# Performance work log

Measured on AMD Instinct MI355X. Metric: run time of the kernel, lower is better.

## Reference

```python
import jax, jax.numpy as jnp
import numpy as np

N_TAXON = 100000
N_SOTU = 200000
D = 128      # input feature dim and hidden_channels
OUT = 64     # out_channels
E_HP = 200000
E_RH = 2000000


def _sage(x_src, x_dst, src, dst, Wl, Wr, b, n_dst):
    # PyG SAGEConv (mean aggr): out = lin_l(mean_{j in N(i)} x_j) + lin_r(x_i)
    msgs = x_src[src]                                            # [E, d] gather
    summed = jax.ops.segment_sum(msgs, dst, num_segments=n_dst)  # [n_dst, d]
    cnt = jax.ops.segment_sum(jnp.ones_like(msgs[:, 0]), dst, num_segments=n_dst)
    mean = summed / jnp.maximum(cnt, 1.0)[:, None]
    return mean @ Wl + b + x_dst @ Wr


def setup_inputs() -> dict:
    key = jax.random.key(0)
    ks = jax.random.split(key, 20)
    s = 1.0 / np.sqrt(D)
    inp = {
        "x_taxon": jax.random.normal(ks[0], (N_TAXON, D), jnp.float32),
        "x_sotu": jax.random.normal(ks[1], (N_SOTU, D), jnp.float32),
        "edge_hp_src": jax.random.randint(ks[2], (E_HP,), 0, N_TAXON),
        "edge_hp_dst": jax.random.randint(ks[3], (E_HP,), 0, N_TAXON),
        "edge_rh_src": jax.random.randint(ks[4], (E_RH,), 0, N_TAXON),
        "edge_rh_dst": jax.random.randint(ks[5], (E_RH,), 0, N_SOTU),
        # conv1: taxon -> taxon
        "W1l": jax.random.normal(ks[6], (D, D), jnp.float32) * s,
        "W1r": jax.random.normal(ks[7], (D, D), jnp.float32) * s,
        "b1": jnp.zeros((D,), jnp.float32),
        # conv2: (taxon, sotu) bipartite
        "W2l": jax.random.normal(ks[8], (D, D), jnp.float32) * s,
        "W2r": jax.random.normal(ks[9], (D, D), jnp.float32) * s,
        "b2": jnp.zeros((D,), jnp.float32),
        # conv3: (taxon_hidden, sotu_hidden) bipartite
        "W3l": jax.random.normal(ks[10], (D, D), jnp.float32) * s,
        "W3r": jax.random.normal(ks[11], (D, D), jnp.float32) * s,
        "b3": jnp.zeros((D,), jnp.float32),
        # final linear
        "Wlin": jax.random.normal(ks[12], (D, OUT), jnp.float32) * s,
        "blin": jnp.zeros((OUT,), jnp.float32),
    }
    return inp


def reference(x_taxon, x_sotu, edge_hp_src, edge_hp_dst, edge_rh_src, edge_rh_dst,
              W1l, W1r, b1, W2l, W2r, b2, W3l, W3r, b3, Wlin, blin):
    taxon_h = jax.nn.relu(_sage(x_taxon, x_taxon, edge_hp_src, edge_hp_dst,
                                W1l, W1r, b1, N_TAXON))
    sotu_h = jax.nn.relu(_sage(x_taxon, x_sotu, edge_rh_src, edge_rh_dst,
                               W2l, W2r, b2, N_SOTU))
    sotu_h = jax.nn.relu(_sage(taxon_h, sotu_h, edge_rh_src, edge_rh_dst,
                               W3l, W3r, b3, N_SOTU))
    return sotu_h @ Wlin + blin
```

## Files before the change

kernel.cpp:

```cpp
#include <hip/hip_runtime.h>
#include <hip/hip_bf16.h>

#define D 128
#define N_TAXON 100000
#define N_SOTU 200000
#define E_HP 200000
#define E_RH 2000000
#define OUTC 64
#define NBUCK 98
#define BSHIFT 11

typedef __hip_bfloat16 bf16;
typedef __bf16 bf16v8 __attribute__((ext_vector_type(8)));
typedef float f32x4 __attribute__((ext_vector_type(4)));
typedef int i32x4 __attribute__((ext_vector_type(4)));
typedef unsigned u32x2 __attribute__((ext_vector_type(2)));

union Frag { i32x4 i; bf16v8 v; };

__device__ __forceinline__ float bflo(unsigned u) { return __uint_as_float(u << 16); }
__device__ __forceinline__ float bfhi(unsigned u) { return __uint_as_float(u & 0xffff0000u); }

__device__ __forceinline__ unsigned short f2bf(float x) {
    unsigned u = __float_as_uint(x);
    unsigned r = (u + 0x7fffu + ((u >> 16) & 1u)) >> 16;
    return (unsigned short)r;
}
__device__ __forceinline__ unsigned packbf(float a, float b) {
    return (unsigned)f2bf(a) | ((unsigned)f2bf(b) << 16);
}

__global__ __launch_bounds__(256) void countAll_kernel(const int* __restrict__ hp_dst,
                                                       const int* __restrict__ rh_dst,
                                                       unsigned* __restrict__ cnt_t,
                                                       unsigned* __restrict__ bcnt)
{
    __shared__ unsigned hist[NBUCK];
    if (threadIdx.x < NBUCK) hist[threadIdx.x] = 0;
    __syncthreads();
    int stride = gridDim.x * 256;
    for (int e = blockIdx.x * 256 + threadIdx.x; e < E_HP; e += stride)
        atomicAdd(&cnt_t[hp_dst[e]], 1u);
    for (int e = blockIdx.x * 256 + threadIdx.x; e < E_RH; e += stride)
        atomicAdd(&hist[rh_dst[e] >> BSHIFT], 1u);
    __syncthreads();
    if (threadIdx.x < NBUCK) atomicAdd(&bcnt[threadIdx.x], hist[threadIdx.x]);
}

__global__ __launch_bounds__(128) void scan98_kernel(const unsigned* __restrict__ bcnt,
                                                     unsigned* __restrict__ bcursor,
                                                     unsigned* __restrict__ bstart,
                                                     unsigned* __restrict__ row_ptr)
{
    __shared__ unsigned v[NBUCK];
    if (threadIdx.x < NBUCK) v[threadIdx.x] = bcnt[threadIdx.x];
    __syncthreads();
    if (threadIdx.x == 0) {
        unsigned acc = 0;
        for (int b = 0; b < NBUCK; ++b) {
            unsigned t = v[b];
            bcursor[b] = acc; bstart[b] = acc; acc += t;
        }
        bstart[NBUCK] = acc;
        row_ptr[N_TAXON + N_SOTU] = E_HP + acc;
    }
}

__global__ __launch_bounds__(256) void partition_kernel(
    const int* __restrict__ src, const int* __restrict__ dst,
    unsigned* __restrict__ bcursor, unsigned long long* __restrict__ ebuf, int n)
{
    __shared__ unsigned hist[NBUCK];
    __shared__ unsigned lcur[NBUCK];
    int base = blockIdx.x * 4096;
    if (threadIdx.x < NBUCK) hist[threadIdx.x] = 0;
    __syncthreads();
    int s[16], d[16];
#pragma unroll
    for (int k = 0; k < 16; ++k) {
        int e = base + k * 256 + threadIdx.x;
        if (e < n) {
            s[k] = src[e]; d[k] = dst[e];
            atomicAdd(&hist[d[k] >> BSHIFT], 1u);
        } else d[k] = -1;
    }
    __syncthreads();
    if (threadIdx.x < NBUCK)
        lcur[threadIdx.x] = atomicAdd(&bcursor[threadIdx.x], hist[threadIdx.x]);
    __syncthreads();
#pragma unroll
    for (int k = 0; k < 16; ++k) {
        if (d[k] >= 0) {
            unsigned slot = atomicAdd(&lcur[d[k] >> BSHIFT], 1u);
            ebuf[slot] = ((unsigned long long)(unsigned)d[k] << 32) | (unsigned)s[k];
        }
    }
}

__global__ __launch_bounds__(256) void scanA_kernel(const unsigned* __restrict__ cnt,
                                                    unsigned* __restrict__ bsum, int n)
{
    int lane = threadIdx.x & 63, wv = threadIdx.x >> 6;
    __shared__ unsigned ws[4];
    int i = blockIdx.x * 256 + threadIdx.x;
    unsigned v = (i < n) ? cnt[i] : 0u;
    for (int off = 1; off < 64; off <<= 1) v += __shfl_xor(v, off, 64);
    if (lane == 0) ws[wv] = v;
    __syncthreads();
    if (threadIdx.x == 0) bsum[blockIdx.x] = ws[0] + ws[1] + ws[2] + ws[3];
}

__global__ __launch_bounds__(1024) void scanB_kernel(unsigned* __restrict__ bsum, int nb,
                                                     unsigned* __restrict__ total_out)
{
    int lane = threadIdx.x & 63, wv = threadIdx.x >> 6;
    __shared__ unsigned wsum[16];
    int t = threadIdx.x;
    unsigned v0 = (2 * t     < nb) ? bsum[2 * t]     : 0u;
    unsigned v1 = (2 * t + 1 < nb) ? bsum[2 * t + 1] : 0u;
    unsigned v = v0 + v1;
    unsigned s = v;
    for (int off = 1; off < 64; off <<= 1) {
        unsigned tt = __shfl_up(s, off, 64);
        if (lane >= off) s += tt;
    }
    if (lane == 63) wsum[wv] = s;
    __syncthreads();
    unsigned woff = 0, tot = 0;
    for (int w = 0; w < 16; ++w) { if (w < wv) woff += wsum[w]; tot += wsum[w]; }
    unsigned ex = woff + s - v;
    if (2 * t     < nb) bsum[2 * t]     = ex;
    if (2 * t + 1 < nb) bsum[2 * t + 1] = ex + v0;
    if (t == 0) *total_out = tot;
}

__global__ __launch_bounds__(256) void scanC_kernel(const unsigned* __restrict__ cnt,
                                                    const unsigned* __restrict__ bsum,
                                                    unsigned* __restrict__ row_ptr,
                                                    unsigned* __restrict__ cursor, int n)
{
    int lane = threadIdx.x & 63, wv = threadIdx.x >> 6;
    __shared__ unsigned wsum[4];
    int i = blockIdx.x * 256 + threadIdx.x;
    unsigned v = (i < n) ? cnt[i] : 0u;
    unsigned s = v;
    for (int off = 1; off < 64; off <<= 1) {
        unsigned t = __shfl_up(s, off, 64);
        if (lane >= off) s += t;
    }
    if (lane == 63) wsum[wv] = s;
    __syncthreads();
    unsigned woff = bsum[blockIdx.x];
    for (int w = 0; w < wv; ++w) woff += wsum[w];
    if (i < n) { unsigned p = woff + s - v; row_ptr[i] = p; cursor[i] = p; }
}

__global__ __launch_bounds__(256) void fill_hp_kernel(const int* __restrict__ src,
                                                      const int* __restrict__ dst,
                                                      unsigned* __restrict__ cursor,
                                                      int* __restrict__ sorted_all)
{
    int stride = gridDim.x * 256;
    for (int i = blockIdx.x * 256 + threadIdx.x; i < E_HP; i += stride) {
        unsigned pos = atomicAdd(&cursor[dst[i]], 1u);
        sorted_all[pos] = src[i];
    }
}

__global__ __launch_bounds__(256) void fillB_kernel(const unsigned long long* __restrict__ ebuf,
                                                    const unsigned* __restrict__ bstart,
                                                    unsigned* __restrict__ row_ptr,
                                                    int* __restrict__ sorted_all)
{
    __shared__ unsigned hist[1 << BSHIFT];
    __shared__ unsigned wsum[4];
    int c = blockIdx.x;
    int dbase = c << BSHIFT;
    for (int i = threadIdx.x; i < (1 << BSHIFT); i += 256) hist[i] = 0;
    __syncthreads();
    unsigned e0 = bstart[c], e1 = bstart[c + 1];
    for (unsigned e = e0 + threadIdx.x; e < e1; e += 256)
        atomicAdd(&hist[(unsigned)(ebuf[e] >> 32) - dbase], 1u);
    __syncthreads();
    int base8 = threadIdx.x * 8;
    unsigned loc[8], s = 0;
#pragma unroll
    for (int i = 0; i < 8; ++i) { loc[i] = s; s += hist[base8 + i]; }
    int lane = threadIdx.x & 63, wv = threadIdx.x >> 6;
    unsigned sc = s;
    for (int off = 1; off < 64; off <<= 1) {
        unsigned t = __shfl_up(sc, off, 64);
        if (lane >= off) sc += t;
    }
    if (lane == 63) wsum[wv] = sc;
    __syncthreads();
    unsigned woff = 0;
    for (int w = 0; w < wv; ++w) woff += wsum[w];
    unsigned tbase = E_HP + e0 + woff + sc - s;
#pragma unroll
    for (int i = 0; i < 8; ++i) {
        int dd = dbase + base8 + i;
        unsigned p = tbase + loc[i];
        if (dd < N_SOTU) row_ptr[N_TAXON + dd] = p;
        hist[base8 + i] = p;
    }
    __syncthreads();
    for (unsigned e = e0 + threadIdx.x; e < e1; e += 256) {
        unsigned long long v = ebuf[e];
        unsigned pos = atomicAdd(&hist[(unsigned)(v >> 32) - dbase], 1u);
        sorted_all[pos] = (int)(unsigned)v;
    }
}

__global__ __launch_bounds__(256) void wprep_all_kernel(
    const float* __restrict__ W1l, const float* __restrict__ W1r,
    const float* __restrict__ W2l, const float* __restrict__ W2r,
    const float* __restrict__ W3l, const float* __restrict__ W3r,
    const float* __restrict__ Wlin, unsigned short* __restrict__ wtbase)
{
    int e = blockIdx.x * 256 + threadIdx.x;
    if (e >= 6 * 16384 + 8192) return;
    const float* srcs[7] = { W1l, W1r, W2l, W2r, W3l, W3r, Wlin };
    int m = e >> 14;
    int local = (m < 6) ? (e & 16383) : (e - 98304);
    int N = (m < 6) ? 128 : 64;
    int k = local / N, col = local - k * N;
    unsigned short* dst = wtbase + ((m < 6) ? m * 16384 : 98304);
    dst[(col * 128 + k) ^ ((col & 7) << 3)] = f2bf(srcs[m][local]);
}

__global__ __launch_bounds__(256) void aggMeanHp_kernel(
    const float* __restrict__ x, const unsigned* __restrict__ rp,
    const int* __restrict__ nbr, unsigned* __restrict__ outm)
{
    int wave = threadIdx.x >> 6, lane = threadIdx.x & 63;
    int bid = (blockIdx.x & 7) * 3125 + (blockIdx.x >> 3);
    int r = bid * 4 + wave;
    unsigned beg = rp[r], end = rp[r + 1];
    float a0 = 0.f, a1 = 0.f;
    unsigned u = beg;
    for (; u + 2 <= end; u += 2) {
        float2 A = ((const float2*)x)[(size_t)nbr[u] * 64 + lane];
        float2 B = ((const float2*)x)[(size_t)nbr[u + 1] * 64 + lane];
        a0 += A.x + B.x; a1 += A.y + B.y;
    }
    if (u < end) {
        float2 A = ((const float2*)x)[(size_t)nbr[u] * 64 + lane];
        a0 += A.x; a1 += A.y;
    }
    unsigned c = end - beg;
    float inv = 1.f / (float)(c ? c : 1u);
    outm[(size_t)r * 64 + lane] = packbf(a0 * inv, a1 * inv);
}

__global__ __launch_bounds__(1024) void gemmTh_kernel(
    const unsigned* __restrict__ A1 , const float* __restrict__ X ,
    const unsigned short* __restrict__ WtA, const unsigned short* __restrict__ WtB,
    const float* __restrict__ bias, unsigned* __restrict__ X2, int M)
{
    __shared__ char sW[65536];
    {
        int tid = threadIdx.x;
        ((i32x4*)sW)[tid]        = ((const i32x4*)WtA)[tid];
        ((i32x4*)sW)[tid + 1024] = ((const i32x4*)WtA)[tid + 1024];
        ((i32x4*)sW)[tid + 2048] = ((const i32x4*)WtB)[tid];
        ((i32x4*)sW)[tid + 3072] = ((const i32x4*)WtB)[tid + 1024];
    }
    __syncthreads();

    int wave = threadIdx.x >> 6, lane = threadIdx.x & 63;
    int ln = lane & 15, g = lane >> 4;
    int row = blockIdx.x * 256 + wave * 16 + ln;
    int rl = row < M ? row : M - 1;
    int swz = (ln & 7) << 4;

    f32x4 acc[8];
#pragma unroll
    for (int cf = 0; cf < 8; ++cf) acc[cf] = ((const f32x4*)bias)[cf * 4 + g];

    const i32x4* a1r = (const i32x4*)(A1 + (size_t)rl * 64);
    const f32x4* xr = (const f32x4*)(X + (size_t)rl * 128);
    unsigned* orow = X2 + (size_t)row * 128;
    i32x4 xpk[4];
#pragma unroll
    for (int ks = 0; ks < 4; ++ks) {
        Frag mf; mf.i = a1r[ks * 4 + g];
        f32x4 fa = xr[ks * 8 + g * 2], fb = xr[ks * 8 + g * 2 + 1];
        Frag xf;
        i32x4 t = { (int)packbf(fa.x, fa.y), (int)packbf(fa.z, fa.w),
                    (int)packbf(fb.x, fb.y), (int)packbf(fb.z, fb.w) };
        xf.i = t; xpk[ks] = t;
#pragma unroll
        for (int cf = 0; cf < 8; ++cf) {
            int off = (((cf * 16 + ln) << 8) + (ks << 6) + (g << 4)) ^ swz;
            Frag wa; wa.i = *(const i32x4*)(sW + off);
            Frag wb; wb.i = *(const i32x4*)(sW + 32768 + off);
            acc[cf] = __builtin_amdgcn_mfma_f32_16x16x32_bf16(wa.v, mf.v, acc[cf], 0, 0, 0);
            acc[cf] = __builtin_amdgcn_mfma_f32_16x16x32_bf16(wb.v, xf.v, acc[cf], 0, 0, 0);
        }
    }

    if (row < M) {
#pragma unroll
        for (int ks = 0; ks < 4; ++ks) {
            int p0 = 16 * ks + 4 * g;
            orow[(p0 + 0) * 2] = (unsigned)xpk[ks][0];
            orow[(p0 + 1) * 2] = (unsigned)xpk[ks][1];
            orow[(p0 + 2) * 2] = (unsigned)xpk[ks][2];
            orow[(p0 + 3) * 2] = (unsigned)xpk[ks][3];
        }
#pragma unroll
        for (int cf = 0; cf < 8; ++cf) {
            int p = cf * 8 + g * 2;
            orow[p * 2 + 1]       = packbf(fmaxf(acc[cf][0], 0.f), fmaxf(acc[cf][1], 0.f));
            orow[(p + 1) * 2 + 1] = packbf(fmaxf(acc[cf][2], 0.f), fmaxf(acc[cf][3], 0.f));
        }
    }
}

__global__ __launch_bounds__(256) void aggMean2_kernel(
    const unsigned* __restrict__ X2, const unsigned* __restrict__ rp,
    const int* __restrict__ nbr,
    unsigned* __restrict__ meanXrh, unsigned* __restrict__ meanH)
{
    int wave = threadIdx.x >> 6, lane = threadIdx.x & 63;
    int bid = (blockIdx.x & 7) * 6250 + (blockIdx.x >> 3);
    int r = bid * 4 + wave;
    unsigned beg = rp[r], end = rp[r + 1];
    float a0 = 0.f, a1 = 0.f, a2 = 0.f, a3 = 0.f;
    unsigned u = beg;
    for (; u + 2 <= end; u += 2) {
        int j0 = nbr[u], j1 = nbr[u + 1];
        u32x2 A = *(const u32x2*)(X2 + (size_t)j0 * 128 + lane * 2);
        u32x2 B = *(const u32x2*)(X2 + (size_t)j1 * 128 + lane * 2);
        a0 += bflo(A.x) + bflo(B.x); a1 += bfhi(A.x) + bfhi(B.x);
        a2 += bflo(A.y) + bflo(B.y); a3 += bfhi(A.y) + bfhi(B.y);
    }
    if (u < end) {
        u32x2 A = *(const u32x2*)(X2 + (size_t)nbr[u] * 128 + lane * 2);
        a0 += bflo(A.x); a1 += bfhi(A.x); a2 += bflo(A.y); a3 += bfhi(A.y);
    }
    unsigned c = end - beg;
    float inv = 1.f / (float)(c ? c : 1u);
    meanXrh[(size_t)r * 64 + lane] = packbf(a0 * inv, a1 * inv);
    meanH[(size_t)r * 64 + lane]   = packbf(a2 * inv, a3 * inv);
}

__global__ __launch_bounds__(1024) void megaTail_kernel(
    const unsigned* __restrict__ meanXrh, const float* __restrict__ xs,
    const unsigned* __restrict__ meanH,
    const unsigned short* __restrict__ Wt2l, const unsigned short* __restrict__ Wt2r,
    const unsigned short* __restrict__ Wt3l, const unsigned short* __restrict__ Wt3r,
    const unsigned short* __restrict__ Wtlin,
    const float* __restrict__ b2, const float* __restrict__ b3,
    const float* __restrict__ blin, float* __restrict__ out, int M)
{
    __shared__ char sW[65536];
    __shared__ unsigned tiles[16 * 1024];
    int tid = threadIdx.x;
    int wave = tid >> 6, lane = tid & 63;
    int ln = lane & 15, g = lane >> 4;
    int row = blockIdx.x * 256 + wave * 16 + ln;
    int rl = row < M ? row : M - 1;
    int swzW = (ln & 7) << 4;
    int swz = (ln & 7) << 2;
    unsigned* tile = tiles + wave * 1024;

    i32x4 w3pre[4], wlpre;
    w3pre[0] = ((const i32x4*)Wt3l)[tid];
    w3pre[1] = ((const i32x4*)Wt3l)[tid + 1024];
    w3pre[2] = ((const i32x4*)Wt3r)[tid];
    w3pre[3] = ((const i32x4*)Wt3r)[tid + 1024];
    wlpre    = ((const i32x4*)Wtlin)[tid];

    ((i32x4*)sW)[tid]        = ((const i32x4*)Wt2l)[tid];
    ((i32x4*)sW)[tid + 1024] = ((const i32x4*)Wt2l)[tid + 1024];
    ((i32x4*)sW)[tid + 2048] = ((const i32x4*)Wt2r)[tid];
    ((i32x4*)sW)[tid + 3072] = ((const i32x4*)Wt2r)[tid + 1024];
    __syncthreads();

    {
        f32x4 acc[8];
#pragma unroll
        for (int cf = 0; cf < 8; ++cf) acc[cf] = ((const f32x4*)b2)[cf * 4 + g];
        const i32x4* a1r = (const i32x4*)(meanXrh + (size_t)rl * 64);
        const f32x4* xr = (const f32x4*)(xs + (size_t)rl * 128);
#pragma unroll
        for (int ks = 0; ks < 4; ++ks) {
            Frag mf; mf.i = a1r[ks * 4 + g];
            f32x4 fa = xr[ks * 8 + g * 2], fb = xr[ks * 8 + g * 2 + 1];
            Frag xf;
            i32x4 t = { (int)packbf(fa.x, fa.y), (int)packbf(fa.z, fa.w),
                        (int)packbf(fb.x, fb.y), (int)packbf(fb.z, fb.w) };
            xf.i = t;
#pragma unroll
            for (int cf = 0; cf < 8; ++cf) {
                int off = (((cf * 16 + ln) << 8) + (ks << 6) + (g << 4)) ^ swzW;
                Frag wa; wa.i = *(const i32x4*)(sW + off);
                Frag wb; wb.i = *(const i32x4*)(sW + 32768 + off);
                acc[cf] = __builtin_amdgcn_mfma_f32_16x16x32_bf16(wa.v, mf.v, acc[cf], 0, 0, 0);
                acc[cf] = __builtin_amdgcn_mfma_f32_16x16x32_bf16(wb.v, xf.v, acc[cf], 0, 0, 0);
            }
        }
#pragma unroll
        for (int cf = 0; cf < 8; ++cf) {
            u32x2 o;
            o.x = packbf(fmaxf(acc[cf][0], 0.f), fmaxf(acc[cf][1], 0.f));
            o.y = packbf(fmaxf(acc[cf][2], 0.f), fmaxf(acc[cf][3], 0.f));
            *(u32x2*)&tile[ln * 64 + ((cf * 8 + g * 2) ^ swz)] = o;
        }
    }

    i32x4 mh[4];
    {
        const i32x4* hr = (const i32x4*)(meanH + (size_t)rl * 64);
#pragma unroll
        for (int ks = 0; ks < 4; ++ks) mh[ks] = hr[ks * 4 + g];
    }
    __syncthreads();
    ((i32x4*)sW)[tid]        = w3pre[0];
    ((i32x4*)sW)[tid + 1024] = w3pre[1];
    ((i32x4*)sW)[tid + 2048] = w3pre[2];
    ((i32x4*)sW)[tid + 3072] = w3pre[3];
    __syncthreads();

    {
        f32x4 acc2[8];
#pragma unroll
        for (int cf = 0; cf < 8; ++cf) acc2[cf] = ((const f32x4*)b3)[cf * 4 + g];
#pragma unroll
        for (int ks = 0; ks < 4; ++ks) {
            Frag mf; mf.i = mh[ks];
            Frag sf; sf.i = *(const i32x4*)&tile[ln * 64 + ((ks * 16 + g * 4) ^ swz)];
#pragma unroll
            for (int cf = 0; cf < 8; ++cf) {
                int off = (((cf * 16 + ln) << 8) + (ks << 6) + (g << 4)) ^ swzW;
                Frag wl; wl.i = *(const i32x4*)(sW + off);
                Frag wr; wr.i = *(const i32x4*)(sW + 32768 + off);
                acc2[cf] = __builtin_amdgcn_mfma_f32_16x16x32_bf16(wl.v, mf.v, acc2[cf], 0, 0, 0);
                acc2[cf] = __builtin_amdgcn_mfma_f32_16x16x32_bf16(wr.v, sf.v, acc2[cf], 0, 0, 0);
            }
        }
#pragma unroll
        for (int cf = 0; cf < 8; ++cf) {
            u32x2 o;
            o.x = packbf(fmaxf(acc2[cf][0], 0.f), fmaxf(acc2[cf][1], 0.f));
            o.y = packbf(fmaxf(acc2[cf][2], 0.f), fmaxf(acc2[cf][3], 0.f));
            *(u32x2*)&tile[ln * 64 + ((cf * 8 + g * 2) ^ swz)] = o;
        }
    }
    __syncthreads();
    ((i32x4*)sW)[tid] = wlpre;
    __syncthreads();

    f32x4 aL[4];
#pragma unroll
    for (int cf = 0; cf < 4; ++cf) aL[cf] = ((const f32x4*)blin)[cf * 4 + g];
#pragma unroll
    for (int ks = 0; ks < 4; ++ks) {
        Frag hf; hf.i = *(const i32x4*)&tile[ln * 64 + ((ks * 16 + g * 4) ^ swz)];
#pragma unroll
        for (int cf = 0; cf < 4; ++cf) {
            int off = (((cf * 16 + ln) << 8) + (ks << 6) + (g << 4)) ^ swzW;
            Frag wf; wf.i = *(const i32x4*)(sW + off);
            aL[cf] = __builtin_amdgcn_mfma_f32_16x16x32_bf16(wf.v, hf.v, aL[cf], 0, 0, 0);
        }
    }
    if (row < M) {
        float* orow = out + (size_t)row * OUTC;
#pragma unroll
        for (int cf = 0; cf < 4; ++cf)
            *(f32x4*)(orow + cf * 16 + g * 4) = aL[cf];
    }
}

extern "C" void kernel_launch(void* const* d_in, const int* in_sizes, int n_in,
                              void* d_out, int out_size, void* d_ws, size_t ws_size,
                              hipStream_t stream)
{
    const float* x_taxon = (const float*)d_in[0];
    const float* x_sotu  = (const float*)d_in[1];
    const int* hp_src = (const int*)d_in[2];
    const int* hp_dst = (const int*)d_in[3];
    const int* rh_src = (const int*)d_in[4];
    const int* rh_dst = (const int*)d_in[5];
    const float* W1l = (const float*)d_in[6];
    const float* W1r = (const float*)d_in[7];
    const float* b1  = (const float*)d_in[8];
    const float* W2l = (const float*)d_in[9];
    const float* W2r = (const float*)d_in[10];
    const float* b2  = (const float*)d_in[11];
    const float* W3l = (const float*)d_in[12];
    const float* W3r = (const float*)d_in[13];
    const float* b3  = (const float*)d_in[14];
    const float* Wlin = (const float*)d_in[15];
    const float* blin = (const float*)d_in[16];
    float* out = (float*)d_out;

    char* ws = (char*)d_ws;
    unsigned* X2      = (unsigned*)(ws);
    unsigned* meanXrh = (unsigned*)(ws + 51200000);
    unsigned* meanH   = (unsigned*)(ws + 102400000);
    unsigned* meanX_hp= (unsigned*)(ws + 153600000);
    unsigned long long* ebuf = (unsigned long long*)(ws + 51200000);
    int*      sorted_all = (int*)(ws + 179200000);
    unsigned* row_ptr = (unsigned*)(ws + 188000000);
    unsigned* cursor  = (unsigned*)(ws + 189200128);
    unsigned* cnt_t   = (unsigned*)(ws + 189600128);
    unsigned* bcnt    = (unsigned*)(ws + 190000128);
    unsigned* bcursor = (unsigned*)(ws + 190000640);
    unsigned* bstart  = (unsigned*)(ws + 190001152);
    unsigned* bsum    = (unsigned*)(ws + 190001664);
    unsigned short* wtbase = (unsigned short*)(ws + 190009856);
    unsigned short* Wt1l = wtbase;
    unsigned short* Wt1r = wtbase + 16384;
    unsigned short* Wt2l = wtbase + 32768;
    unsigned short* Wt2r = wtbase + 49152;
    unsigned short* Wt3l = wtbase + 65536;
    unsigned short* Wt3r = wtbase + 81920;
    unsigned short* Wtlin = wtbase + 98304;

    hipMemsetAsync(cnt_t, 0, 100000 * 4 + 512, stream);

    countAll_kernel<<<256, 256, 0, stream>>>(hp_dst, rh_dst, cnt_t, bcnt);
    scan98_kernel<<<1, 128, 0, stream>>>(bcnt, bcursor, bstart, row_ptr);
    partition_kernel<<<(E_RH + 4095) / 4096, 256, 0, stream>>>(rh_src, rh_dst, bcursor, ebuf, E_RH);
    {
        int nb = (N_TAXON + 255) / 256;
        scanA_kernel<<<nb, 256, 0, stream>>>(cnt_t, bsum, N_TAXON);
        scanB_kernel<<<1, 1024, 0, stream>>>(bsum, nb, row_ptr + N_TAXON);
        scanC_kernel<<<nb, 256, 0, stream>>>(cnt_t, bsum, row_ptr, cursor, N_TAXON);
    }
    fill_hp_kernel<<<782, 256, 0, stream>>>(hp_src, hp_dst, cursor, sorted_all);
    fillB_kernel<<<NBUCK, 256, 0, stream>>>(ebuf, bstart, row_ptr, sorted_all);

    wprep_all_kernel<<<(6 * 16384 + 8192 + 255) / 256, 256, 0, stream>>>(
        W1l, W1r, W2l, W2r, W3l, W3r, Wlin, wtbase);

    aggMeanHp_kernel<<<N_TAXON / 4, 256, 0, stream>>>(x_taxon, row_ptr, sorted_all, meanX_hp);

    gemmTh_kernel<<<(N_TAXON + 255) / 256, 1024, 0, stream>>>(
        meanX_hp, x_taxon, Wt1l, Wt1r, b1, X2, N_TAXON);

    aggMean2_kernel<<<N_SOTU / 4, 256, 0, stream>>>(
        X2, row_ptr + N_TAXON, sorted_all, meanXrh, meanH);

    megaTail_kernel<<<(N_SOTU + 255) / 256, 1024, 0, stream>>>(
        meanXrh, x_sotu, meanH, Wt2l, Wt2r, Wt3l, Wt3r, Wtlin, b2, b3, blin, out, N_SOTU);
}
```

Measured before the change: 458.7 us.

## Unify CSR build for both edge sets and fuse hp mean aggregation into GEMM

Builds one bucketed CSR over all 300k destination nodes, so the hp edges go through the same partition/fillB path as the rh edges. This removes the per-node atomic count, the three-kernel scan and the atomic fill kernel. The hp mean aggregation now runs inside the first GEMM kernel, writing swizzled bf16 tiles to shared memory instead of a global meanX buffer. This saves several launches and a global round trip. In exchange, the gemm kernel uses 64KB+64KB of LDS, which limits occupancy, and each wave gathers 16 rows serially before its MFMA work.

```diff
diff --git a/kernel.cpp b/kernel.cpp
--- a/kernel.cpp
+++ b/kernel.cpp
@@ -4,10 +4,12 @@
 #define D 128
 #define N_TAXON 100000
 #define N_SOTU 200000
+#define N_ALL 300000
 #define E_HP 200000
 #define E_RH 2000000
+#define E_ALL 2200000
 #define OUTC 64
-#define NBUCK 98
+#define NBUCK 147
 #define BSHIFT 11
 
 typedef __hip_bfloat16 bf16;
@@ -32,61 +34,61 @@
 
 __global__ __launch_bounds__(256) void countAll_kernel(const int* __restrict__ hp_dst,
                                                        const int* __restrict__ rh_dst,
-                                                       unsigned* __restrict__ cnt_t,
                                                        unsigned* __restrict__ bcnt)
 {
     __shared__ unsigned hist[NBUCK];
-    if (threadIdx.x < NBUCK) hist[threadIdx.x] = 0;
+    for (int i = threadIdx.x; i < NBUCK; i += 256) hist[i] = 0;
     __syncthreads();
     int stride = gridDim.x * 256;
     for (int e = blockIdx.x * 256 + threadIdx.x; e < E_HP; e += stride)
-        atomicAdd(&cnt_t[hp_dst[e]], 1u);
+        atomicAdd(&hist[hp_dst[e] >> BSHIFT], 1u);
     for (int e = blockIdx.x * 256 + threadIdx.x; e < E_RH; e += stride)
-        atomicAdd(&hist[rh_dst[e] >> BSHIFT], 1u);
-    __syncthreads();
-    if (threadIdx.x < NBUCK) atomicAdd(&bcnt[threadIdx.x], hist[threadIdx.x]);
-}
-
-__global__ __launch_bounds__(128) void scan98_kernel(const unsigned* __restrict__ bcnt,
-                                                     unsigned* __restrict__ bcursor,
-                                                     unsigned* __restrict__ bstart,
-                                                     unsigned* __restrict__ row_ptr)
-{
-    __shared__ unsigned v[NBUCK];
-    if (threadIdx.x < NBUCK) v[threadIdx.x] = bcnt[threadIdx.x];
-    __syncthreads();
+        atomicAdd(&hist[(N_TAXON + rh_dst[e]) >> BSHIFT], 1u);
+    __syncthreads();
+    for (int i = threadIdx.x; i < NBUCK; i += 256) atomicAdd(&bcnt[i], hist[i]);
+}
+
+__global__ __launch_bounds__(256) void scanB147_kernel(const unsigned* __restrict__ bcnt,
+                                                       unsigned* __restrict__ bcursor,
+                                                       unsigned* __restrict__ bstart,
+                                                       unsigned* __restrict__ row_ptr)
+{
     if (threadIdx.x == 0) {
         unsigned acc = 0;
         for (int b = 0; b < NBUCK; ++b) {
-            unsigned t = v[b];
+            unsigned t = bcnt[b];
             bcursor[b] = acc; bstart[b] = acc; acc += t;
         }
         bstart[NBUCK] = acc;
-        row_ptr[N_TAXON + N_SOTU] = E_HP + acc;
+        row_ptr[N_ALL] = E_ALL;
     }
 }
 
 __global__ __launch_bounds__(256) void partition_kernel(
-    const int* __restrict__ src, const int* __restrict__ dst,
-    unsigned* __restrict__ bcursor, unsigned long long* __restrict__ ebuf, int n)
+    const int* __restrict__ hp_src, const int* __restrict__ hp_dst,
+    const int* __restrict__ rh_src, const int* __restrict__ rh_dst,
+    unsigned* __restrict__ bcursor, unsigned long long* __restrict__ ebuf)
 {
     __shared__ unsigned hist[NBUCK];
     __shared__ unsigned lcur[NBUCK];
     int base = blockIdx.x * 4096;
-    if (threadIdx.x < NBUCK) hist[threadIdx.x] = 0;
+    for (int i = threadIdx.x; i < NBUCK; i += 256) hist[i] = 0;
     __syncthreads();
     int s[16], d[16];
 #pragma unroll
     for (int k = 0; k < 16; ++k) {
         int e = base + k * 256 + threadIdx.x;
-        if (e < n) {
-            s[k] = src[e]; d[k] = dst[e];
+        if (e < E_HP) {
+            s[k] = hp_src[e]; d[k] = hp_dst[e];
+            atomicAdd(&hist[d[k] >> BSHIFT], 1u);
+        } else if (e < E_ALL) {
+            s[k] = rh_src[e - E_HP]; d[k] = N_TAXON + rh_dst[e - E_HP];
             atomicAdd(&hist[d[k] >> BSHIFT], 1u);
         } else d[k] = -1;
     }
     __syncthreads();
-    if (threadIdx.x < NBUCK)
-        lcur[threadIdx.x] = atomicAdd(&bcursor[threadIdx.x], hist[threadIdx.x]);
+    for (int i = threadIdx.x; i < NBUCK; i += 256)
+        lcur[i] = atomicAdd(&bcursor[i], hist[i]);
     __syncthreads();
 #pragma unroll
     for (int k = 0; k < 16; ++k) {
@@ -94,76 +96,6 @@
             unsigned slot = atomicAdd(&lcur[d[k] >> BSHIFT], 1u);
             ebuf[slot] = ((unsigned long long)(unsigned)d[k] << 32) | (unsigned)s[k];
         }
-    }
-}
-
-__global__ __launch_bounds__(256) void scanA_kernel(const unsigned* __restrict__ cnt,
-                                                    unsigned* __restrict__ bsum, int n)
-{
-    int lane = threadIdx.x & 63, wv = threadIdx.x >> 6;
-    __shared__ unsigned ws[4];
-    int i = blockIdx.x * 256 + threadIdx.x;
-    unsigned v = (i < n) ? cnt[i] : 0u;
-    for (int off = 1; off < 64; off <<= 1) v += __shfl_xor(v, off, 64);
-    if (lane == 0) ws[wv] = v;
-    __syncthreads();
-    if (threadIdx.x == 0) bsum[blockIdx.x] = ws[0] + ws[1] + ws[2] + ws[3];
-}
-
-__global__ __launch_bounds__(1024) void scanB_kernel(unsigned* __restrict__ bsum, int nb,
-                                                     unsigned* __restrict__ total_out)
-{
-    int lane = threadIdx.x & 63, wv = threadIdx.x >> 6;
-    __shared__ unsigned wsum[16];
-    int t = threadIdx.x;
-    unsigned v0 = (2 * t     < nb) ? bsum[2 * t]     : 0u;
-    unsigned v1 = (2 * t + 1 < nb) ? bsum[2 * t + 1] : 0u;
-    unsigned v = v0 + v1;
-    unsigned s = v;
-    for (int off = 1; off < 64; off <<= 1) {
-        unsigned tt = __shfl_up(s, off, 64);
-        if (lane >= off) s += tt;
-    }
-    if (lane == 63) wsum[wv] = s;
-    __syncthreads();
-    unsigned woff = 0, tot = 0;
-    for (int w = 0; w < 16; ++w) { if (w < wv) woff += wsum[w]; tot += wsum[w]; }
-    unsigned ex = woff + s - v;
-    if (2 * t     < nb) bsum[2 * t]     = ex;
-    if (2 * t + 1 < nb) bsum[2 * t + 1] = ex + v0;
-    if (t == 0) *total_out = tot;
-}
-
-__global__ __launch_bounds__(256) void scanC_kernel(const unsigned* __restrict__ cnt,
-                                                    const unsigned* __restrict__ bsum,
-                                                    unsigned* __restrict__ row_ptr,
-                                                    unsigned* __restrict__ cursor, int n)
-{
-    int lane = threadIdx.x & 63, wv = threadIdx.x >> 6;
-    __shared__ unsigned wsum[4];
-    int i = blockIdx.x * 256 + threadIdx.x;
-    unsigned v = (i < n) ? cnt[i] : 0u;
-    unsigned s = v;
-    for (int off = 1; off < 64; off <<= 1) {
-        unsigned t = __shfl_up(s, off, 64);
-        if (lane >= off) s += t;
-    }
-    if (lane == 63) wsum[wv] = s;
-    __syncthreads();
-    unsigned woff = bsum[blockIdx.x];
-    for (int w = 0; w < wv; ++w) woff += wsum[w];
-    if (i < n) { unsigned p = woff + s - v; row_ptr[i] = p; cursor[i] = p; }
-}
-
-__global__ __launch_bounds__(256) void fill_hp_kernel(const int* __restrict__ src,
-                                                      const int* __restrict__ dst,
-                                                      unsigned* __restrict__ cursor,
-                                                      int* __restrict__ sorted_all)
-{
-    int stride = gridDim.x * 256;
-    for (int i = blockIdx.x * 256 + threadIdx.x; i < E_HP; i += stride) {
-        unsigned pos = atomicAdd(&cursor[dst[i]], 1u);
-        sorted_all[pos] = src[i];
     }
 }
 
@@ -196,12 +128,12 @@
     __syncthreads();
     unsigned woff = 0;
     for (int w = 0; w < wv; ++w) woff += wsum[w];
-    unsigned tbase = E_HP + e0 + woff + sc - s;
+    unsigned tbase = e0 + woff + sc - s;
 #pragma unroll
     for (int i = 0; i < 8; ++i) {
         int dd = dbase + base8 + i;
         unsigned p = tbase + loc[i];
-        if (dd < N_SOTU) row_ptr[N_TAXON + dd] = p;
+        if (dd < N_ALL) row_ptr[dd] = p;
         hist[base8 + i] = p;
     }
     __syncthreads();
@@ -229,62 +161,63 @@
     dst[(col * 128 + k) ^ ((col & 7) << 3)] = f2bf(srcs[m][local]);
 }
 
-__global__ __launch_bounds__(256) void aggMeanHp_kernel(
-    const float* __restrict__ x, const unsigned* __restrict__ rp,
-    const int* __restrict__ nbr, unsigned* __restrict__ outm)
-{
-    int wave = threadIdx.x >> 6, lane = threadIdx.x & 63;
-    int bid = (blockIdx.x & 7) * 3125 + (blockIdx.x >> 3);
-    int r = bid * 4 + wave;
-    unsigned beg = rp[r], end = rp[r + 1];
-    float a0 = 0.f, a1 = 0.f;
-    unsigned u = beg;
-    for (; u + 2 <= end; u += 2) {
-        float2 A = ((const float2*)x)[(size_t)nbr[u] * 64 + lane];
-        float2 B = ((const float2*)x)[(size_t)nbr[u + 1] * 64 + lane];
-        a0 += A.x + B.x; a1 += A.y + B.y;
-    }
-    if (u < end) {
-        float2 A = ((const float2*)x)[(size_t)nbr[u] * 64 + lane];
-        a0 += A.x; a1 += A.y;
-    }
-    unsigned c = end - beg;
-    float inv = 1.f / (float)(c ? c : 1u);
-    outm[(size_t)r * 64 + lane] = packbf(a0 * inv, a1 * inv);
-}
-
-__global__ __launch_bounds__(1024) void gemmTh_kernel(
-    const unsigned* __restrict__ A1 , const float* __restrict__ X ,
+__global__ __launch_bounds__(1024) void gemmTh2_kernel(
+    const float* __restrict__ X ,
+    const unsigned* __restrict__ rp, const int* __restrict__ nbr,
     const unsigned short* __restrict__ WtA, const unsigned short* __restrict__ WtB,
     const float* __restrict__ bias, unsigned* __restrict__ X2, int M)
 {
     __shared__ char sW[65536];
-    {
-        int tid = threadIdx.x;
-        ((i32x4*)sW)[tid]        = ((const i32x4*)WtA)[tid];
-        ((i32x4*)sW)[tid + 1024] = ((const i32x4*)WtA)[tid + 1024];
-        ((i32x4*)sW)[tid + 2048] = ((const i32x4*)WtB)[tid];
-        ((i32x4*)sW)[tid + 3072] = ((const i32x4*)WtB)[tid + 1024];
-    }
-    __syncthreads();
-
-    int wave = threadIdx.x >> 6, lane = threadIdx.x & 63;
+    __shared__ unsigned tiles[16 * 1024];
+    int tid = threadIdx.x;
+    ((i32x4*)sW)[tid]        = ((const i32x4*)WtA)[tid];
+    ((i32x4*)sW)[tid + 1024] = ((const i32x4*)WtA)[tid + 1024];
+    ((i32x4*)sW)[tid + 2048] = ((const i32x4*)WtB)[tid];
+    ((i32x4*)sW)[tid + 3072] = ((const i32x4*)WtB)[tid + 1024];
+
+    int wave = tid >> 6, lane = tid & 63;
     int ln = lane & 15, g = lane >> 4;
-    int row = blockIdx.x * 256 + wave * 16 + ln;
+    int rbase = blockIdx.x * 256 + wave * 16;
+    unsigned* tile = tiles + wave * 1024;
+
+    for (int i = 0; i < 16; ++i) {
+        int r = rbase + i;
+        float a0 = 0.f, a1 = 0.f;
+        if (r < M) {
+            unsigned beg = rp[r], end = rp[r + 1];
+            unsigned u = beg;
+            for (; u + 2 <= end; u += 2) {
+                float2 A = ((const float2*)X)[(size_t)nbr[u] * 64 + lane];
+                float2 B = ((const float2*)X)[(size_t)nbr[u + 1] * 64 + lane];
+                a0 += A.x + B.x; a1 += A.y + B.y;
+            }
+            if (u < end) {
+                float2 A = ((const float2*)X)[(size_t)nbr[u] * 64 + lane];
+                a0 += A.x; a1 += A.y;
+            }
+            unsigned cdeg = end - beg;
+            float inv = 1.f / (float)(cdeg ? cdeg : 1u);
+            a0 *= inv; a1 *= inv;
+        }
+        tile[i * 64 + (lane ^ ((i & 7) << 2))] = packbf(a0, a1);
+    }
+    __syncthreads();
+
+    int row = rbase + ln;
     int rl = row < M ? row : M - 1;
-    int swz = (ln & 7) << 4;
+    int swzW = (ln & 7) << 4;
+    int swz = (ln & 7) << 2;
 
     f32x4 acc[8];
 #pragma unroll
     for (int cf = 0; cf < 8; ++cf) acc[cf] = ((const f32x4*)bias)[cf * 4 + g];
 
-    const i32x4* a1r = (const i32x4*)(A1 + (size_t)rl * 64);
     const f32x4* xr = (const f32x4*)(X + (size_t)rl * 128);
     unsigned* orow = X2 + (size_t)row * 128;
     i32x4 xpk[4];
 #pragma unroll
     for (int ks = 0; ks < 4; ++ks) {
-        Frag mf; mf.i = a1r[ks * 4 + g];
+        Frag mf; mf.i = *(const i32x4*)&tile[ln * 64 + ((ks * 16 + g * 4) ^ swz)];
         f32x4 fa = xr[ks * 8 + g * 2], fb = xr[ks * 8 + g * 2 + 1];
         Frag xf;
         i32x4 t = { (int)packbf(fa.x, fa.y), (int)packbf(fa.z, fa.w),
@@ -292,7 +225,7 @@
         xf.i = t; xpk[ks] = t;
 #pragma unroll
         for (int cf = 0; cf < 8; ++cf) {
-            int off = (((cf * 16 + ln) << 8) + (ks << 6) + (g << 4)) ^ swz;
+            int off = (((cf * 16 + ln) << 8) + (ks << 6) + (g << 4)) ^ swzW;
             Frag wa; wa.i = *(const i32x4*)(sW + off);
             Frag wb; wb.i = *(const i32x4*)(sW + 32768 + off);
             acc[cf] = __builtin_amdgcn_mfma_f32_16x16x32_bf16(wa.v, mf.v, acc[cf], 0, 0, 0);
@@ -501,17 +434,13 @@
     unsigned* X2      = (unsigned*)(ws);
     unsigned* meanXrh = (unsigned*)(ws + 51200000);
     unsigned* meanH   = (unsigned*)(ws + 102400000);
-    unsigned* meanX_hp= (unsigned*)(ws + 153600000);
     unsigned long long* ebuf = (unsigned long long*)(ws + 51200000);
     int*      sorted_all = (int*)(ws + 179200000);
     unsigned* row_ptr = (unsigned*)(ws + 188000000);
-    unsigned* cursor  = (unsigned*)(ws + 189200128);
-    unsigned* cnt_t   = (unsigned*)(ws + 189600128);
-    unsigned* bcnt    = (unsigned*)(ws + 190000128);
-    unsigned* bcursor = (unsigned*)(ws + 190000640);
-    unsigned* bstart  = (unsigned*)(ws + 190001152);
-    unsigned* bsum    = (unsigned*)(ws + 190001664);
-    unsigned short* wtbase = (unsigned short*)(ws + 190009856);
+    unsigned* bcnt    = (unsigned*)(ws + 189200128);
+    unsigned* bcursor = (unsigned*)(ws + 189200768);
+    unsigned* bstart  = (unsigned*)(ws + 189201408);
+    unsigned short* wtbase = (unsigned short*)(ws + 189202048);
     unsigned short* Wt1l = wtbase;
     unsigned short* Wt1r = wtbase + 16384;
     unsigned short* Wt2l = wtbase + 32768;
@@ -520,27 +449,19 @@
     unsigned short* Wt3r = wtbase + 81920;
     unsigned short* Wtlin = wtbase + 98304;
 
-    hipMemsetAsync(cnt_t, 0, 100000 * 4 + 512, stream);
-
-    countAll_kernel<<<256, 256, 0, stream>>>(hp_dst, rh_dst, cnt_t, bcnt);
-    scan98_kernel<<<1, 128, 0, stream>>>(bcnt, bcursor, bstart, row_ptr);
-    partition_kernel<<<(E_RH + 4095) / 4096, 256, 0, stream>>>(rh_src, rh_dst, bcursor, ebuf, E_RH);
-    {
-        int nb = (N_TAXON + 255) / 256;
-        scanA_kernel<<<nb, 256, 0, stream>>>(cnt_t, bsum, N_TAXON);
-        scanB_kernel<<<1, 1024, 0, stream>>>(bsum, nb, row_ptr + N_TAXON);
-        scanC_kernel<<<nb, 256, 0, stream>>>(cnt_t, bsum, row_ptr, cursor, N_TAXON);
-    }
-    fill_hp_kernel<<<782, 256, 0, stream>>>(hp_src, hp_dst, cursor, sorted_all);
+    hipMemsetAsync(bcnt, 0, 640, stream);
+
+    countAll_kernel<<<512, 256, 0, stream>>>(hp_dst, rh_dst, bcnt);
+    scanB147_kernel<<<1, 256, 0, stream>>>(bcnt, bcursor, bstart, row_ptr);
+    partition_kernel<<<(E_ALL + 4095) / 4096, 256, 0, stream>>>(
+        hp_src, hp_dst, rh_src, rh_dst, bcursor, ebuf);
     fillB_kernel<<<NBUCK, 256, 0, stream>>>(ebuf, bstart, row_ptr, sorted_all);
 
     wprep_all_kernel<<<(6 * 16384 + 8192 + 255) / 256, 256, 0, stream>>>(
         W1l, W1r, W2l, W2r, W3l, W3r, Wlin, wtbase);
 
-    aggMeanHp_kernel<<<N_TAXON / 4, 256, 0, stream>>>(x_taxon, row_ptr, sorted_all, meanX_hp);
-
-    gemmTh_kernel<<<(N_TAXON + 255) / 256, 1024, 0, stream>>>(
-        meanX_hp, x_taxon, Wt1l, Wt1r, b1, X2, N_TAXON);
+    gemmTh2_kernel<<<(N_TAXON + 255) / 256, 1024, 0, stream>>>(
+        x_taxon, row_ptr, sorted_all, Wt1l, Wt1r, b1, X2, N_TAXON);
 
     aggMean2_kernel<<<N_SOTU / 4, 256, 0, stream>>>(
         X2, row_ptr + N_TAXON, sorted_all, meanXrh, meanH);
```

Result: faster. 445.0 us (median of 3 runs) (-3.0%).
